# Kernel optimization log

Measured on AMD Instinct MI355X. Metric: run time of the kernel, lower is better.

## Reference

```python
import jax, jax.numpy as jnp
import numpy as np

N = 10000      # nodes
E = 320000     # edges (before self-loops)
IN = 128       # input features
HID = 32       # hidden channels per head
HEADS = 8
OUT = 40       # classes
NEG_SLOPE = 0.2  # PyG GATConv leaky_relu slope


def gat_conv(x, W, a_src, a_dst, b, src, dst, n, concat):
    """One PyG-style GATConv (eval mode, self-loops already in src/dst)."""
    H, C = a_src.shape
    xp = (x @ W).reshape(n, H, C)                       # [N,H,C]
    al_s = jnp.einsum('nhc,hc->nh', xp, a_src)          # [N,H]
    al_d = jnp.einsum('nhc,hc->nh', xp, a_dst)          # [N,H]
    e = jax.nn.leaky_relu(al_s[src] + al_d[dst], NEG_SLOPE)  # [E,H]
    # segment softmax over incoming edges of each dst node
    m = jax.ops.segment_max(e, dst, num_segments=n)
    ee = jnp.exp(e - m[dst])
    s = jax.ops.segment_sum(ee, dst, num_segments=n)
    alpha = ee / (s[dst] + 1e-16)                       # [E,H]
    out = jax.ops.segment_sum(alpha[:, :, None] * xp[src], dst, num_segments=n)  # [N,H,C]
    out = out.reshape(n, H * C) if concat else out.mean(axis=1)
    return out + b


def setup_inputs() -> dict:
    key = jax.random.key(0)
    ks = jax.random.split(key, 16)
    p = lambda k, shape: (jax.random.normal(k, shape, jnp.float32) * 0.1)
    HC = HEADS * HID
    return {
        'x': jax.random.normal(ks[0], (N, IN), jnp.float32),
        'edge_index': jax.random.randint(ks[1], (2, E), 0, N),
        'W1': p(ks[2], (IN, HC)), 'a_src1': p(ks[3], (HEADS, HID)), 'a_dst1': p(ks[4], (HEADS, HID)), 'b1': jnp.zeros((HC,), jnp.float32),
        'W2': p(ks[5], (HC, HC)), 'a_src2': p(ks[6], (HEADS, HID)), 'a_dst2': p(ks[7], (HEADS, HID)), 'b2': jnp.zeros((HC,), jnp.float32),
        'W3': p(ks[8], (HC, OUT)), 'a_src3': p(ks[9], (1, OUT)), 'a_dst3': p(ks[10], (1, OUT)), 'b3': jnp.zeros((OUT,), jnp.float32),
    }


def reference(x, edge_index, W1, a_src1, a_dst1, b1, W2, a_src2, a_dst2, b2,
              W3, a_src3, a_dst3, b3):
    n = x.shape[0]
    loop = jnp.arange(n, dtype=edge_index.dtype)
    src = jnp.concatenate([edge_index[0], loop])   # PyG add_self_loops=True
    dst = jnp.concatenate([edge_index[1], loop])
    h = jax.nn.elu(gat_conv(x, W1, a_src1, a_dst1, b1, src, dst, n, True))
    h = jax.nn.elu(gat_conv(h, W2, a_src2, a_dst2, b2, src, dst, n, True))
    h = gat_conv(h, W3, a_src3, a_dst3, b3, src, dst, n, False)
    return jax.nn.log_softmax(h, axis=1)
```

## Files before the change

### kernel.cpp

```cpp
#include <hip/hip_runtime.h>
#include <hip/hip_bf16.h>
#include <math.h>


#define DEV_INLINE __device__ __forceinline__

typedef __attribute__((ext_vector_type(8))) short short8;
typedef __attribute__((ext_vector_type(4))) float f32x4;
typedef __attribute__((ext_vector_type(2))) float f32x2;
typedef unsigned short ushort_t;
typedef unsigned int uint_t;
typedef unsigned char uchar_t;

#define ELLW 128

#if defined(__has_builtin)
#if __has_builtin(__builtin_amdgcn_cvt_pk_f32_fp8) && __has_builtin(__builtin_amdgcn_cvt_pk_fp8_f32)
#define FP8_HW 1
#endif
#endif
#ifndef FP8_HW
#define FP8_HW 0
#endif

DEV_INLINE float leaky02(float x) { return x > 0.f ? x : 0.2f * x; }
DEV_INLINE float elu1(float x) { return x > 0.f ? x : expm1f(x); }

DEV_INLINE ushort_t f2bf(float f) {
    uint_t u = __float_as_uint(f);
    u += 0x7FFFu + ((u >> 16) & 1u);
    return (ushort_t)(u >> 16);
}
DEV_INLINE float bf2f(ushort_t u) { return __uint_as_float(((uint_t)u) << 16); }


DEV_INLINE uint_t f2fp8(float v) {
#if FP8_HW
    return __builtin_amdgcn_cvt_pk_fp8_f32(v, v, 0, false) & 0xFFu;
#else
    float a = fabsf(v);
    uint_t s = (__float_as_uint(v) >> 24) & 0x80u;
    if (!(a >= 0.0009765625f)) return s;
    if (a >= 448.f) return s | 0x7Eu;
    if (a < 0.015625f) {
        int m = (int)(a * 512.f + 0.5f);
        if (m >= 8) return s | 0x08u;
        return s | (uint_t)m;
    }
    uint_t ab = __float_as_uint(a);
    uint_t r = ab + 0x0007FFFFu + ((ab >> 20) & 1u);
    uint_t e = (r >> 23) - 127u + 7u;
    uint_t m = (r >> 20) & 7u;
    if (e > 15u || (e == 15u && m == 7u)) return s | 0x7Eu;
    return s | (e << 3) | m;
#endif
}

DEV_INLINE void fp8x8_dec(uint2 w, float* f) {
#if FP8_HW
    f32x2 a0 = __builtin_amdgcn_cvt_pk_f32_fp8((int)w.x, false);
    f32x2 a1 = __builtin_amdgcn_cvt_pk_f32_fp8((int)w.x, true);
    f32x2 a2 = __builtin_amdgcn_cvt_pk_f32_fp8((int)w.y, false);
    f32x2 a3 = __builtin_amdgcn_cvt_pk_f32_fp8((int)w.y, true);
    f[0] = a0.x; f[1] = a0.y; f[2] = a1.x; f[3] = a1.y;
    f[4] = a2.x; f[5] = a2.y; f[6] = a3.x; f[7] = a3.y;
#else
    uint_t b[8] = {w.x & 255u, (w.x >> 8) & 255u, (w.x >> 16) & 255u, w.x >> 24,
                   w.y & 255u, (w.y >> 8) & 255u, (w.y >> 16) & 255u, w.y >> 24};
#pragma unroll
    for (int i = 0; i < 8; ++i) {
        uint_t em = b[i] & 0x7Fu;
        float mag = (em >= 8u) ? __uint_as_float(0x3C000000u + (em << 20))
                               : (float)(int)em * 0.001953125f;
        f[i] = (b[i] & 0x80u) ? -mag : mag;
    }
#endif
}


__global__ void prep_kernel(const float* __restrict__ W1, ushort_t* __restrict__ W1T,
                            const float* __restrict__ W2, ushort_t* __restrict__ W2T,
                            const float* __restrict__ W3, ushort_t* __restrict__ W3T,
                            const float* __restrict__ as1, const float* __restrict__ ad1,
                            const float* __restrict__ as2, const float* __restrict__ ad2,
                            const float* __restrict__ as3, const float* __restrict__ ad3,
                            int* __restrict__ cursor, int n) {
    int i = blockIdx.x * blockDim.x + threadIdx.x;
    if (i < n) { cursor[i] = 0; return; }
    i -= n;
    if (i < 128 * 256) {
        int k = i >> 8, c = i & 255;
        W1T[(size_t)c * 128 + k] = f2bf(W1[i]);
        return;
    }
    i -= 128 * 256;
    if (i < 256 * 256) {
        int k = i >> 8, c = i & 255;
        W2T[(size_t)c * 256 + k] = f2bf(W2[i]);
        return;
    }
    i -= 256 * 256;
    if (i < 256 * 40) {
        int k = i / 40, c = i - k * 40;
        W3T[(size_t)c * 256 + k] = f2bf(W3[i]);
        return;
    }
    i -= 256 * 40;
    if (i < 1024) {
        int h = i >> 7, k = i & 127;
        float acc = 0.f;
#pragma unroll
        for (int c = 0; c < 32; ++c) acc += W1[k * 256 + h * 32 + c] * as1[h * 32 + c];
        W1T[(size_t)(256 + h) * 128 + k] = f2bf(acc);
        return;
    }
    i -= 1024;
    if (i < 1024) {
        int h = i >> 7, k = i & 127;
        float acc = 0.f;
#pragma unroll
        for (int c = 0; c < 32; ++c) acc += W1[k * 256 + h * 32 + c] * ad1[h * 32 + c];
        W1T[(size_t)(264 + h) * 128 + k] = f2bf(acc);
        return;
    }
    i -= 1024;
    if (i < 2048) {
        int h = i >> 8, k = i & 255;
        float acc = 0.f;
#pragma unroll
        for (int c = 0; c < 32; ++c) acc += W2[k * 256 + h * 32 + c] * as2[h * 32 + c];
        W2T[(size_t)(256 + h) * 256 + k] = f2bf(acc);
        return;
    }
    i -= 2048;
    if (i < 2048) {
        int h = i >> 8, k = i & 255;
        float acc = 0.f;
#pragma unroll
        for (int c = 0; c < 32; ++c) acc += W2[k * 256 + h * 32 + c] * ad2[h * 32 + c];
        W2T[(size_t)(264 + h) * 256 + k] = f2bf(acc);
        return;
    }
    i -= 2048;
    if (i < 256) {
        float acc = 0.f;
#pragma unroll
        for (int c = 0; c < 40; ++c) acc += W3[i * 40 + c] * as3[c];
        W3T[(size_t)40 * 256 + i] = f2bf(acc);
        return;
    }
    i -= 256;
    if (i < 256) {
        float acc = 0.f;
#pragma unroll
        for (int c = 0; c < 40; ++c) acc += W3[i * 40 + c] * ad3[c];
        W3T[(size_t)41 * 256 + i] = f2bf(acc);
        return;
    }
}


DEV_INLINE int lds_slot(int r, int c) { return r * 4 + ((c + (r >> 1)) & 3); }

DEV_INLINE void gemm_body(ushort_t* __restrict__ As, ushort_t* __restrict__ Bs,
                          const ushort_t* __restrict__ A, const ushort_t* __restrict__ BT,
                          ushort_t* __restrict__ Cbf, uchar_t* __restrict__ C8,
                          float* __restrict__ ALS, float* __restrict__ ALD,
                          int M, int NOUT, int NH, int NTOT, int K, int bx, int by) {
    const int tid = threadIdx.x;
    const int wave = tid >> 6, lane = tid & 63;
    const int row0 = by * 64;
    const int col0 = bx * 64;

    const int sr = tid >> 2, sc = tid & 3;
    const int a_row = row0 + sr;
    const int b_row = col0 + sr;

    const int fr = lane & 15;
    const int fc = lane >> 4;

    f32x4 acc0 = {}, acc1 = {}, acc2 = {}, acc3 = {};

    for (int k0 = 0; k0 < K; k0 += 32) {
        short8 av = {}, bv = {};
        if (a_row < M) av = *(const short8*)(A + (size_t)a_row * K + k0 + sc * 8);
        if (b_row < NTOT) bv = *(const short8*)(BT + (size_t)b_row * K + k0 + sc * 8);
        __syncthreads();
        *(short8*)(As + lds_slot(sr, sc) * 8) = av;
        *(short8*)(Bs + lds_slot(sr, sc) * 8) = bv;
        __syncthreads();

        const int arow = wave * 16 + fr;
        short8 afrag = *(const short8*)(As + lds_slot(arow, fc) * 8);
        short8 b0 = *(const short8*)(Bs + lds_slot(0 * 16 + fr, fc) * 8);
        short8 b1 = *(const short8*)(Bs + lds_slot(1 * 16 + fr, fc) * 8);
        short8 b2 = *(const short8*)(Bs + lds_slot(2 * 16 + fr, fc) * 8);
        short8 b3 = *(const short8*)(Bs + lds_slot(3 * 16 + fr, fc) * 8);
        acc0 = __builtin_amdgcn_mfma_f32_16x16x32_bf16(afrag, b0, acc0, 0, 0, 0);
        acc1 = __builtin_amdgcn_mfma_f32_16x16x32_bf16(afrag, b1, acc1, 0, 0, 0);
        acc2 = __builtin_amdgcn_mfma_f32_16x16x32_bf16(afrag, b2, acc2, 0, 0, 0);
        acc3 = __builtin_amdgcn_mfma_f32_16x16x32_bf16(afrag, b3, acc3, 0, 0, 0);
    }
    __syncthreads();

    const int crow = row0 + wave * 16 + (lane >> 4) * 4;
    const int ccol = col0 + (lane & 15);
    f32x4 accs[4] = {acc0, acc1, acc2, acc3};
#pragma unroll
    for (int ct = 0; ct < 4; ++ct) {
        int col = ccol + ct * 16;
#pragma unroll
        for (int j = 0; j < 4; ++j) {
            int row = crow + j;
            if (row >= M) continue;
            float v = accs[ct][j];
            if (col < NOUT) {
                if (C8) C8[(size_t)row * NOUT + col] = (uchar_t)f2fp8(v);
                else    Cbf[(size_t)row * NOUT + col] = f2bf(v);
            } else {
                int cc = col - NOUT;
                if (cc < NH) ALS[(size_t)row * NH + cc] = v;
                else if (cc < 2 * NH) ALD[(size_t)row * NH + (cc - NH)] = v;
            }
        }
    }
}

DEV_INLINE void gemm1_body(ushort_t* __restrict__ As, ushort_t* __restrict__ Bs,
                           const float* __restrict__ X, const ushort_t* __restrict__ BT,
                           uchar_t* __restrict__ C8, float* __restrict__ ALS,
                           float* __restrict__ ALD, int M, int bx, int by) {
    const int tid = threadIdx.x;
    const int wave = tid >> 6, lane = tid & 63;
    const int row0 = by * 64;
    const int col0 = bx * 64;

    const int sr = tid >> 2, sc = tid & 3;
    const int a_row = row0 + sr;
    const int b_row = col0 + sr;

    const int fr = lane & 15;
    const int fc = lane >> 4;

    f32x4 acc0 = {}, acc1 = {}, acc2 = {}, acc3 = {};

    for (int k0 = 0; k0 < 128; k0 += 32) {
        short8 av = {}, bv = {};
        if (a_row < M) {
            const float* xp = X + (size_t)a_row * 128 + k0 + sc * 8;
            float4 f0 = *(const float4*)(xp);
            float4 f1 = *(const float4*)(xp + 4);
            av[0] = (short)f2bf(f0.x); av[1] = (short)f2bf(f0.y);
            av[2] = (short)f2bf(f0.z); av[3] = (short)f2bf(f0.w);
            av[4] = (short)f2bf(f1.x); av[5] = (short)f2bf(f1.y);
            av[6] = (short)f2bf(f1.z); av[7] = (short)f2bf(f1.w);
        }
        if (b_row < 272) bv = *(const short8*)(BT + (size_t)b_row * 128 + k0 + sc * 8);
        __syncthreads();
        *(short8*)(As + lds_slot(sr, sc) * 8) = av;
        *(short8*)(Bs + lds_slot(sr, sc) * 8) = bv;
        __syncthreads();

        const int arow = wave * 16 + fr;
        short8 afrag = *(const short8*)(As + lds_slot(arow, fc) * 8);
        short8 b0 = *(const short8*)(Bs + lds_slot(0 * 16 + fr, fc) * 8);
        short8 b1 = *(const short8*)(Bs + lds_slot(1 * 16 + fr, fc) * 8);
        short8 b2 = *(const short8*)(Bs + lds_slot(2 * 16 + fr, fc) * 8);
        short8 b3 = *(const short8*)(Bs + lds_slot(3 * 16 + fr, fc) * 8);
        acc0 = __builtin_amdgcn_mfma_f32_16x16x32_bf16(afrag, b0, acc0, 0, 0, 0);
        acc1 = __builtin_amdgcn_mfma_f32_16x16x32_bf16(afrag, b1, acc1, 0, 0, 0);
        acc2 = __builtin_amdgcn_mfma_f32_16x16x32_bf16(afrag, b2, acc2, 0, 0, 0);
        acc3 = __builtin_amdgcn_mfma_f32_16x16x32_bf16(afrag, b3, acc3, 0, 0, 0);
    }
    __syncthreads();

    const int crow = row0 + wave * 16 + (lane >> 4) * 4;
    const int ccol = col0 + (lane & 15);
    f32x4 accs[4] = {acc0, acc1, acc2, acc3};
#pragma unroll
    for (int ct = 0; ct < 4; ++ct) {
        int col = ccol + ct * 16;
#pragma unroll
        for (int j = 0; j < 4; ++j) {
            int row = crow + j;
            if (row >= M) continue;
            float v = accs[ct][j];
            if (col < 256) {
                C8[(size_t)row * 256 + col] = (uchar_t)f2fp8(v);
            } else {
                int cc = col - 256;
                if (cc < 8) ALS[(size_t)row * 8 + cc] = v;
                else if (cc < 16) ALD[(size_t)row * 8 + (cc - 8)] = v;
            }
        }
    }
}

__global__ __launch_bounds__(256) void gemm_kernel(const ushort_t* __restrict__ A,
                                                   const ushort_t* __restrict__ BT,
                                                   ushort_t* __restrict__ Cbf,
                                                   uchar_t* __restrict__ C8,
                                                   float* __restrict__ ALS,
                                                   float* __restrict__ ALD,
                                                   int M, int NOUT, int NH, int NTOT,
                                                   int K, int gx) {
    __shared__ ushort_t As[64 * 32];
    __shared__ ushort_t Bs[64 * 32];
    gemm_body(As, Bs, A, BT, Cbf, C8, ALS, ALD, M, NOUT, NH, NTOT, K,
              blockIdx.x % gx, blockIdx.x / gx);
}

__global__ __launch_bounds__(256) void scatter_gemm1_kernel(const int* __restrict__ src,
                                                            const int* __restrict__ dst,
                                                            int* __restrict__ cursor,
                                                            int* __restrict__ ell, int e,
                                                            int svb,
                                                            const float* __restrict__ X,
                                                            const ushort_t* __restrict__ BT,
                                                            uchar_t* __restrict__ C8,
                                                            float* __restrict__ ALS,
                                                            float* __restrict__ ALD,
                                                            int M, int gx) {
    __shared__ ushort_t As[64 * 32];
    __shared__ ushort_t Bs[64 * 32];
    if (blockIdx.x < svb) {
        int i = blockIdx.x * 256 + threadIdx.x;
        if (i < e) {
            int d = dst[i];
            int p = atomicAdd(&cursor[d], 1);
            ell[d * ELLW + p] = src[i];
        }
        return;
    }
    int b = blockIdx.x - svb;
    gemm1_body(As, Bs, X, BT, C8, ALS, ALD, M, b % gx, b / gx);
}


__global__ __launch_bounds__(256) void aggregate_h8_kernel(const uchar_t* __restrict__ xp8,
                                                           const float* __restrict__ als,
                                                           const float* __restrict__ ald,
                                                           const int* __restrict__ degv,
                                                           const int* __restrict__ ell,
                                                           const float* __restrict__ bias,
                                                           ushort_t* __restrict__ out, int n) {
    int node = (blockIdx.x * blockDim.x + threadIdx.x) >> 6;
    int lane = threadIdx.x & 63;
    if (node >= n) return;
    const int half = lane >> 5;
    const int lh = lane & 31;
    const int ch = lh * 8;
    const int head = lh >> 2;
    const int deg = degv[node];
    const int rs = node * ELLW, re = rs + deg;
    const float ad = ald[node * 8 + head];
    const float m = leaky02(als[node * 8 + head] + ad);

    float acc[8];
    float ssum;
    if (half == 0) {
        uint2 sv = *(const uint2*)(xp8 + (size_t)node * 256 + ch);
        float sf[8];
        fp8x8_dec(sv, sf);
#pragma unroll
        for (int i = 0; i < 8; ++i) acc[i] = sf[i];
        ssum = 1.0f;
    } else {
#pragma unroll
        for (int i = 0; i < 8; ++i) acc[i] = 0.f;
        ssum = 0.f;
    }

    for (int base = rs; base < re; base += 64) {
        const int cnt = (re - base < 64) ? (re - base) : 64;
        int myi = (lane < cnt) ? ell[base + lane] : 0;
        int j = 0;
        for (; j + 8 <= cnt; j += 8) {
            int s0 = __shfl(myi, j + half);
            int s1 = __shfl(myi, j + 2 + half);
            int s2 = __shfl(myi, j + 4 + half);
            int s3 = __shfl(myi, j + 6 + half);
            float a0 = als[s0 * 8 + head];
            float a1 = als[s1 * 8 + head];
            float a2 = als[s2 * 8 + head];
            float a3 = als[s3 * 8 + head];
            uint2 v0 = *(const uint2*)(xp8 + (size_t)s0 * 256 + ch);
            uint2 v1 = *(const uint2*)(xp8 + (size_t)s1 * 256 + ch);
            uint2 v2 = *(const uint2*)(xp8 + (size_t)s2 * 256 + ch);
            uint2 v3 = *(const uint2*)(xp8 + (size_t)s3 * 256 + ch);
            float p0 = __expf(leaky02(a0 + ad) - m);
            float p1 = __expf(leaky02(a1 + ad) - m);
            float p2 = __expf(leaky02(a2 + ad) - m);
            float p3 = __expf(leaky02(a3 + ad) - m);
            ssum += (p0 + p1) + (p2 + p3);
            float f0[8], f1[8], f2[8], f3[8];
            fp8x8_dec(v0, f0);
            fp8x8_dec(v1, f1);
            fp8x8_dec(v2, f2);
            fp8x8_dec(v3, f3);
#pragma unroll
            for (int i = 0; i < 8; ++i)
                acc[i] += (p0 * f0[i] + p1 * f1[i]) + (p2 * f2[i] + p3 * f3[i]);
        }
        for (; j < cnt; j += 2) {
            int jj = j + half;
            int s = __shfl(myi, jj & 63);
            bool valid = jj < cnt;
            float a = als[s * 8 + head];
            uint2 v = *(const uint2*)(xp8 + (size_t)s * 256 + ch);
            float p = valid ? __expf(leaky02(a + ad) - m) : 0.f;
            ssum += p;
            float fv[8];
            fp8x8_dec(v, fv);
#pragma unroll
            for (int i = 0; i < 8; ++i) acc[i] += p * fv[i];
        }
    }

    ssum += __shfl_xor(ssum, 32);
#pragma unroll
    for (int i = 0; i < 8; ++i) acc[i] += __shfl_xor(acc[i], 32);

    if (half == 0) {
        float inv = 1.f / ssum;
        float4 ba = *(const float4*)(bias + ch);
        float4 bb = *(const float4*)(bias + ch + 4);
        float bv[8] = {ba.x, ba.y, ba.z, ba.w, bb.x, bb.y, bb.z, bb.w};
        short8 o;
#pragma unroll
        for (int i = 0; i < 8; ++i) o[i] = (short)f2bf(elu1(acc[i] * inv + bv[i]));
        *(short8*)(out + (size_t)node * 256 + ch) = o;
    }
}


__global__ __launch_bounds__(256) void aggregate_out_kernel(const ushort_t* __restrict__ xp,
                                                            const float* __restrict__ als,
                                                            const float* __restrict__ ald,
                                                            const int* __restrict__ degv,
                                                            const int* __restrict__ ell,
                                                            const float* __restrict__ bias,
                                                            float* __restrict__ out, int n) {
    int node = (blockIdx.x * blockDim.x + threadIdx.x) >> 6;
    int lane = threadIdx.x & 63;
    if (node >= n) return;
    const int half = lane >> 5;
    const int lh = lane & 31;
    const bool act = lh < 20;
    const int ch = lh * 2;
    const int deg = degv[node];
    const int rs = node * ELLW, re = rs + deg;
    const float ad = ald[node];
    const float m = leaky02(als[node] + ad);

    float a0, a1, ssum;
    if (half == 0) {
        if (act) {
            ushort2 sv = *(const ushort2*)(xp + (size_t)node * 40 + ch);
            a0 = bf2f(sv.x); a1 = bf2f(sv.y);
        } else { a0 = a1 = 0.f; }
        ssum = 1.0f;
    } else { a0 = a1 = 0.f; ssum = 0.f; }

    for (int base = rs; base < re; base += 64) {
        const int cnt = (re - base < 64) ? (re - base) : 64;
        int myi = (lane < cnt) ? ell[base + lane] : 0;
        int j = 0;
        for (; j + 8 <= cnt; j += 8) {
            int s0 = __shfl(myi, j + half);
            int s1 = __shfl(myi, j + 2 + half);
            int s2 = __shfl(myi, j + 4 + half);
            int s3 = __shfl(myi, j + 6 + half);
            float e0 = als[s0];
            float e1 = als[s1];
            float e2 = als[s2];
            float e3 = als[s3];
            ushort2 v0 = act ? *(const ushort2*)(xp + (size_t)s0 * 40 + ch) : ushort2{0, 0};
            ushort2 v1 = act ? *(const ushort2*)(xp + (size_t)s1 * 40 + ch) : ushort2{0, 0};
            ushort2 v2 = act ? *(const ushort2*)(xp + (size_t)s2 * 40 + ch) : ushort2{0, 0};
            ushort2 v3 = act ? *(const ushort2*)(xp + (size_t)s3 * 40 + ch) : ushort2{0, 0};
            float p0 = __expf(leaky02(e0 + ad) - m);
            float p1 = __expf(leaky02(e1 + ad) - m);
            float p2 = __expf(leaky02(e2 + ad) - m);
            float p3 = __expf(leaky02(e3 + ad) - m);
            ssum += (p0 + p1) + (p2 + p3);
            a0 += (p0 * bf2f(v0.x) + p1 * bf2f(v1.x)) + (p2 * bf2f(v2.x) + p3 * bf2f(v3.x));
            a1 += (p0 * bf2f(v0.y) + p1 * bf2f(v1.y)) + (p2 * bf2f(v2.y) + p3 * bf2f(v3.y));
        }
        for (; j < cnt; j += 2) {
            int jj = j + half;
            int s = __shfl(myi, jj & 63);
            bool valid = jj < cnt;
            float a = als[s];
            ushort2 v = act ? *(const ushort2*)(xp + (size_t)s * 40 + ch) : ushort2{0, 0};
            float p = valid ? __expf(leaky02(a + ad) - m) : 0.f;
            ssum += p;
            a0 += p * bf2f(v.x);
            a1 += p * bf2f(v.y);
        }
    }

    ssum += __shfl_xor(ssum, 32);
    a0 += __shfl_xor(a0, 32);
    a1 += __shfl_xor(a1, 32);

    float inv = 1.f / ssum;
    float2 b2 = act ? *(const float2*)(bias + ch) : float2{0.f, 0.f};
    float o0 = act ? (a0 * inv + b2.x) : -INFINITY;
    float o1 = act ? (a1 * inv + b2.y) : -INFINITY;

    float mx = fmaxf(o0, o1);
#pragma unroll
    for (int off = 16; off >= 1; off >>= 1) mx = fmaxf(mx, __shfl_xor(mx, off));
    float ex = act ? (__expf(o0 - mx) + __expf(o1 - mx)) : 0.f;
#pragma unroll
    for (int off = 16; off >= 1; off >>= 1) ex += __shfl_xor(ex, off);
    float lse = mx + __logf(ex);
    if (half == 0 && act) {
        float2 o = {o0 - lse, o1 - lse};
        *(float2*)(out + (size_t)node * 40 + ch) = o;
    }
}


extern "C" void kernel_launch(void* const* d_in, const int* in_sizes, int n_in,
                              void* d_out, int out_size, void* d_ws, size_t ws_size,
                              hipStream_t stream) {
    const float* x      = (const float*)d_in[0];
    const int*   edge   = (const int*)d_in[1];
    const float* W1     = (const float*)d_in[2];
    const float* a_src1 = (const float*)d_in[3];
    const float* a_dst1 = (const float*)d_in[4];
    const float* b1     = (const float*)d_in[5];
    const float* W2     = (const float*)d_in[6];
    const float* a_src2 = (const float*)d_in[7];
    const float* a_dst2 = (const float*)d_in[8];
    const float* b2     = (const float*)d_in[9];
    const float* W3     = (const float*)d_in[10];
    const float* a_src3 = (const float*)d_in[11];
    const float* a_dst3 = (const float*)d_in[12];
    const float* b3     = (const float*)d_in[13];
    float* out = (float*)d_out;

    const int n = in_sizes[0] / 128;
    const int e = in_sizes[1] / 2;

    char* ws = (char*)d_ws;
    size_t off = 0;
    auto alloc = [&](size_t bytes) -> void* {
        void* p = ws + off;
        off += (bytes + 255) & ~(size_t)255;
        return p;
    };
    uchar_t*  xp8       = (uchar_t*)alloc((size_t)n * 256);
    ushort_t* h_bf      = (ushort_t*)alloc((size_t)n * 256 * 2);
    ushort_t* xp3       = (ushort_t*)alloc((size_t)n * 40 * 2);
    ushort_t* W1T       = (ushort_t*)alloc((size_t)272 * 128 * 2);
    ushort_t* W2T       = (ushort_t*)alloc((size_t)272 * 256 * 2);
    ushort_t* W3T       = (ushort_t*)alloc((size_t)42 * 256 * 2);
    float*    als       = (float*)alloc((size_t)n * 8 * 4);
    float*    ald       = (float*)alloc((size_t)n * 8 * 4);
    int*      cursor    = (int*)alloc((size_t)n * 4);
    int*      ell       = (int*)alloc((size_t)n * ELLW * 4);
    (void)ws_size;

    const int* srcs = edge;
    const int* dsts = edge + e;

    const int mby = (n + 63) / 64;
    const int svb = (e + 255) / 256;

    {
        int prep_total = n + 128 * 256 + 256 * 256 + 256 * 40
                       + 1024 + 1024 + 2048 + 2048 + 256 + 256;
        prep_kernel<<<(prep_total + 255) / 256, 256, 0, stream>>>(
            W1, W1T, W2, W2T, W3, W3T,
            a_src1, a_dst1, a_src2, a_dst2, a_src3, a_dst3, cursor, n);
    }
    scatter_gemm1_kernel<<<svb + 5 * mby, 256, 0, stream>>>(
        srcs, dsts, cursor, ell, e, svb, x, W1T, xp8, als, ald, n, 5);

    const int agg_grid = (n * 64 + 255) / 256;

    aggregate_h8_kernel<<<agg_grid, 256, 0, stream>>>(xp8, als, ald, cursor, ell, b1, h_bf, n);
    gemm_kernel<<<5 * mby, 256, 0, stream>>>(h_bf, W2T, nullptr, xp8, als, ald,
                                             n, 256, 8, 272, 256, 5);
    aggregate_h8_kernel<<<agg_grid, 256, 0, stream>>>(xp8, als, ald, cursor, ell, b2, h_bf, n);
    gemm_kernel<<<1 * mby, 256, 0, stream>>>(h_bf, W3T, xp3, nullptr, als, ald,
                                             n, 40, 1, 42, 256, 1);
    aggregate_out_kernel<<<agg_grid, 256, 0, stream>>>(xp3, als, ald, cursor, ell, b3, out, n);
}
```

Before: 101.9 us.

## Fuse layer-3 projection GEMM into layer-2 aggregation epilogue

The second aggregation kernel now multiplies each node's ELU output by W3T directly (with attention-logit columns) using per-lane dot products and wave shuffle reductions. Each half-wave handles 21 of the 42 output columns. This removes the third GEMM launch and the write and reread of the 256-wide bf16 hidden tensor. In exchange, every wave does 21 shuffle-reduction rounds and reloads W3T rows from cache, where the MFMA GEMM did this work on matrix cores. Layer-3 logits go to separate als3/ald3 buffers.

After: 101.5 us. No clear change (-0.4%).

```diff
diff --git a/kernel.cpp b/kernel.cpp
--- a/kernel.cpp
+++ b/kernel.cpp
@@ -164,7 +164,7 @@
 
 DEV_INLINE void gemm_body(ushort_t* __restrict__ As, ushort_t* __restrict__ Bs,
                           const ushort_t* __restrict__ A, const ushort_t* __restrict__ BT,
-                          ushort_t* __restrict__ Cbf, uchar_t* __restrict__ C8,
+                          uchar_t* __restrict__ C8,
                           float* __restrict__ ALS, float* __restrict__ ALD,
                           int M, int NOUT, int NH, int NTOT, int K, int bx, int by) {
     const int tid = threadIdx.x;
@@ -215,8 +215,7 @@
             if (row >= M) continue;
             float v = accs[ct][j];
             if (col < NOUT) {
-                if (C8) C8[(size_t)row * NOUT + col] = (uchar_t)f2fp8(v);
-                else    Cbf[(size_t)row * NOUT + col] = f2bf(v);
+                C8[(size_t)row * NOUT + col] = (uchar_t)f2fp8(v);
             } else {
                 int cc = col - NOUT;
                 if (cc < NH) ALS[(size_t)row * NH + cc] = v;
@@ -298,7 +297,6 @@
 
 __global__ __launch_bounds__(256) void gemm_kernel(const ushort_t* __restrict__ A,
                                                    const ushort_t* __restrict__ BT,
-                                                   ushort_t* __restrict__ Cbf,
                                                    uchar_t* __restrict__ C8,
                                                    float* __restrict__ ALS,
                                                    float* __restrict__ ALD,
@@ -306,7 +304,7 @@
                                                    int K, int gx) {
     __shared__ ushort_t As[64 * 32];
     __shared__ ushort_t Bs[64 * 32];
-    gemm_body(As, Bs, A, BT, Cbf, C8, ALS, ALD, M, NOUT, NH, NTOT, K,
+    gemm_body(As, Bs, A, BT, C8, ALS, ALD, M, NOUT, NH, NTOT, K,
               blockIdx.x % gx, blockIdx.x / gx);
 }
 
@@ -337,13 +335,19 @@
 }
 
 
+template <int FUSE3>
 __global__ __launch_bounds__(256) void aggregate_h8_kernel(const uchar_t* __restrict__ xp8,
                                                            const float* __restrict__ als,
                                                            const float* __restrict__ ald,
                                                            const int* __restrict__ degv,
                                                            const int* __restrict__ ell,
                                                            const float* __restrict__ bias,
-                                                           ushort_t* __restrict__ out, int n) {
+                                                           ushort_t* __restrict__ out,
+                                                           const ushort_t* __restrict__ W3T,
+                                                           ushort_t* __restrict__ xp3,
+                                                           float* __restrict__ als3,
+                                                           float* __restrict__ ald3,
+                                                           int n) {
     int node = (blockIdx.x * blockDim.x + threadIdx.x) >> 6;
     int lane = threadIdx.x & 63;
     if (node >= n) return;
@@ -421,15 +425,48 @@
 #pragma unroll
     for (int i = 0; i < 8; ++i) acc[i] += __shfl_xor(acc[i], 32);
 
-    if (half == 0) {
+    if (FUSE3 == 0) {
+        if (half == 0) {
+            float inv = 1.f / ssum;
+            float4 ba = *(const float4*)(bias + ch);
+            float4 bb = *(const float4*)(bias + ch + 4);
+            float bv[8] = {ba.x, ba.y, ba.z, ba.w, bb.x, bb.y, bb.z, bb.w};
+            short8 o;
+#pragma unroll
+            for (int i = 0; i < 8; ++i) o[i] = (short)f2bf(elu1(acc[i] * inv + bv[i]));
+            *(short8*)(out + (size_t)node * 256 + ch) = o;
+        }
+    } else {
         float inv = 1.f / ssum;
         float4 ba = *(const float4*)(bias + ch);
         float4 bb = *(const float4*)(bias + ch + 4);
         float bv[8] = {ba.x, ba.y, ba.z, ba.w, bb.x, bb.y, bb.z, bb.w};
-        short8 o;
-#pragma unroll
-        for (int i = 0; i < 8; ++i) o[i] = (short)f2bf(elu1(acc[i] * inv + bv[i]));
-        *(short8*)(out + (size_t)node * 256 + ch) = o;
+        float hf[8];
+#pragma unroll
+        for (int i = 0; i < 8; ++i) hf[i] = elu1(acc[i] * inv + bv[i]);
+
+        float res = 0.f;
+#pragma unroll
+        for (int idx = 0; idx < 21; ++idx) {
+            int c = half * 21 + idx;
+            short8 w = *(const short8*)(W3T + (size_t)c * 256 + ch);
+            float p = hf[0] * bf2f((ushort_t)w[0]) + hf[1] * bf2f((ushort_t)w[1])
+                    + hf[2] * bf2f((ushort_t)w[2]) + hf[3] * bf2f((ushort_t)w[3])
+                    + hf[4] * bf2f((ushort_t)w[4]) + hf[5] * bf2f((ushort_t)w[5])
+                    + hf[6] * bf2f((ushort_t)w[6]) + hf[7] * bf2f((ushort_t)w[7]);
+            p += __shfl_xor(p, 1);
+            p += __shfl_xor(p, 2);
+            p += __shfl_xor(p, 4);
+            p += __shfl_xor(p, 8);
+            p += __shfl_xor(p, 16);
+            if (lh == idx) res = p;
+        }
+        if (lh < 21) {
+            int c = half * 21 + lh;
+            if (c < 40)      xp3[(size_t)node * 40 + c] = f2bf(res);
+            else if (c == 40) als3[node] = res;
+            else             ald3[node] = res;
+        }
     }
 }
 
@@ -560,6 +597,8 @@
     ushort_t* W3T       = (ushort_t*)alloc((size_t)42 * 256 * 2);
     float*    als       = (float*)alloc((size_t)n * 8 * 4);
     float*    ald       = (float*)alloc((size_t)n * 8 * 4);
+    float*    als3      = (float*)alloc((size_t)n * 4);
+    float*    ald3      = (float*)alloc((size_t)n * 4);
     int*      cursor    = (int*)alloc((size_t)n * 4);
     int*      ell       = (int*)alloc((size_t)n * ELLW * 4);
     (void)ws_size;
@@ -582,11 +621,11 @@
 
     const int agg_grid = (n * 64 + 255) / 256;
 
-    aggregate_h8_kernel<<<agg_grid, 256, 0, stream>>>(xp8, als, ald, cursor, ell, b1, h_bf, n);
-    gemm_kernel<<<5 * mby, 256, 0, stream>>>(h_bf, W2T, nullptr, xp8, als, ald,
+    aggregate_h8_kernel<0><<<agg_grid, 256, 0, stream>>>(
+        xp8, als, ald, cursor, ell, b1, h_bf, nullptr, nullptr, nullptr, nullptr, n);
+    gemm_kernel<<<5 * mby, 256, 0, stream>>>(h_bf, W2T, xp8, als, ald,
                                              n, 256, 8, 272, 256, 5);
-    aggregate_h8_kernel<<<agg_grid, 256, 0, stream>>>(xp8, als, ald, cursor, ell, b2, h_bf, n);
-    gemm_kernel<<<1 * mby, 256, 0, stream>>>(h_bf, W3T, xp3, nullptr, als, ald,
-                                             n, 40, 1, 42, 256, 1);
-    aggregate_out_kernel<<<agg_grid, 256, 0, stream>>>(xp3, als, ald, cursor, ell, b3, out, n);
-}
+    aggregate_h8_kernel<1><<<agg_grid, 256, 0, stream>>>(
+        xp8, als, ald, cursor, ell, b2, nullptr, W3T, xp3, als3, ald3, n);
+    aggregate_out_kernel<<<agg_grid, 256, 0, stream>>>(xp3, als3, ald3, cursor, ell, b3, out, n);
+}
```
